# Performance work log

Measured on AMD Instinct MI355X. Metric: run time of the kernel, lower is better.

Reference implementation:

```python
import jax, jax.numpy as jnp
import numpy as np


def setup_inputs() -> dict:
    key = jax.random.key(0)
    x = jax.random.normal(key, (16, 2048, 64), dtype=jnp.float32)
    return {"x": x, "pred_len": 720, "k": 16, "low_freq": 1}


def reference(x, pred_len, k, low_freq):
    # x: (b, t, d); t assumed even (matches torch branch x_freq[:, low_freq:-1])
    b, t, d = x.shape
    x_freq = jnp.fft.rfft(x, axis=1)[:, low_freq:-1]          # (b, F, d) complex
    f = jnp.fft.rfftfreq(t).astype(jnp.float32)[low_freq:-1]  # (F,)

    # top-k frequencies per (batch, channel) by magnitude
    mag = jnp.transpose(jnp.abs(x_freq), (0, 2, 1))           # (b, d, F)
    _, idx = jax.lax.top_k(mag, k)                            # (b, d, k)
    xf_sel = jnp.take_along_axis(jnp.transpose(x_freq, (0, 2, 1)), idx, axis=2)
    xf_sel = jnp.transpose(xf_sel, (0, 2, 1))                 # (b, k, d)
    f_sel = jnp.transpose(f[idx], (0, 2, 1))                  # (b, k, d)

    # extrapolate: append conjugate / negated-frequency pairs
    xf = jnp.concatenate([xf_sel, jnp.conj(xf_sel)], axis=1)  # (b, 2k, d)
    ff = jnp.concatenate([f_sel, -f_sel], axis=1)[:, :, None, :]   # (b, 2k, 1, d)
    t_val = jnp.arange(t + pred_len, dtype=jnp.float32)[None, None, :, None]
    amp = (jnp.abs(xf) / t)[:, :, None, :]                    # (b, 2k, 1, d)
    phase = jnp.angle(xf)[:, :, None, :]                      # (b, 2k, 1, d)
    x_time = amp * jnp.cos(2.0 * jnp.pi * ff * t_val + phase) # (b, 2k, t+pred_len, d)
    return x_time.sum(axis=1)                                 # (b, t+pred_len, d)
```

## Files before the change

### kernel.cpp

```cpp
#include <hip/hip_runtime.h>
#include <hip/hip_bf16.h>

#define B_SZ 16
#define T_SZ 2048
#define D_SZ 64
#define M_SZ 1024
#define K_SEL 16
#define TOUT 2768
#define TPT 8
#define TAUS_PER_BLOCK (4 * TPT)
#define NCHUNK ((TOUT + TAUS_PER_BLOCK - 1) / TAUS_PER_BLOCK)

__global__ __launch_bounds__(256) void transpose_kernel(
    const float* __restrict__ x, float* __restrict__ xT)
{
    __shared__ float tile[64][65];
    const int b    = blockIdx.y;
    const int t0   = blockIdx.x * 64;
    const int lane = threadIdx.x & 63;
    const int row4 = threadIdx.x >> 6;

    #pragma unroll
    for (int rr = 0; rr < 16; ++rr) {
        int r = rr * 4 + row4;
        tile[r][lane] = x[((size_t)b * T_SZ + t0 + r) * D_SZ + lane];
    }
    __syncthreads();
    #pragma unroll
    for (int rr = 0; rr < 16; ++rr) {
        int d = rr * 4 + row4;
        xT[((size_t)b * D_SZ + d) * T_SZ + t0 + lane] = tile[lane][d];
    }
}

__global__ __launch_bounds__(256) void fft_topk_kernel(
    const float* __restrict__ xT,
    int* __restrict__ sel_j,
    float* __restrict__ sel_re,
    float* __restrict__ sel_im)
{
    __shared__ float a_re[M_SZ], a_im[M_SZ];
    __shared__ float tw_re[M_SZ / 2], tw_im[M_SZ / 2];
    __shared__ float X_re[M_SZ], X_im[M_SZ];
    __shared__ float mag2[M_SZ];
    __shared__ float cand_v[64];
    __shared__ int   cand_j[64];

    const int bd   = blockIdx.x;
    const int tid  = threadIdx.x;
    const int lane = tid & 63;
    const int w    = tid >> 6;

    for (int k = tid; k < M_SZ / 2; k += 256) {
        float a = (float)k * (1.0f / 512.0f);
        tw_re[k] =  cospif(a);
        tw_im[k] = -sinpif(a);
    }

    const float2* xb2 = (const float2*)(xT + (size_t)bd * T_SZ);
    #pragma unroll
    for (int r = 0; r < 4; ++r) {
        int m = tid + 256 * r;
        float2 v = xb2[m];
        int pos = __brev((unsigned)m) >> 22;
        a_re[pos] = v.x;
        a_im[pos] = v.y;
    }
    __syncthreads();

    for (int s = 0; s < 10; ++s) {
        #pragma unroll 2
        for (int q = tid; q < M_SZ / 2; q += 256) {
            int half = 1 << s;
            int pos  = q & (half - 1);
            int i0   = ((q >> s) << (s + 1)) + pos;
            int i1   = i0 + half;
            int twi  = pos << (9 - s);
            float wr = tw_re[twi], wi = tw_im[twi];
            float br = a_re[i1],  bi = a_im[i1];
            float tr = fmaf(wr, br, -wi * bi);
            float ti = fmaf(wr, bi,  wi * br);
            float ar = a_re[i0],  ai = a_im[i0];
            a_re[i0] = ar + tr;  a_im[i0] = ai + ti;
            a_re[i1] = ar - tr;  a_im[i1] = ai - ti;
        }
        __syncthreads();
    }

    for (int j = tid; j < M_SZ; j += 256) {
        if (j == 0) {
            X_re[0] = 0.0f; X_im[0] = 0.0f; mag2[0] = -2.0f;
            continue;
        }
        int jc = M_SZ - j;
        float zr = a_re[j],  zi = a_im[j];
        float cr = a_re[jc], ci = a_im[jc];
        float er = 0.5f * (zr + cr), ei = 0.5f * (zi - ci);
        float ur = zr - cr,  vv = zi + ci;
        float orr = 0.5f * vv, oii = -0.5f * ur;
        float a  = (float)j * (1.0f / 1024.0f);
        float twr =  cospif(a);
        float twq = -sinpif(a);
        float xr = er + twr * orr - twq * oii;
        float xi = ei + twr * oii + twq * orr;
        X_re[j] = xr; X_im[j] = xi;
        mag2[j] = xr * xr + xi * xi;
    }
    __syncthreads();

    float v[4]; int jj[4];
    #pragma unroll
    for (int r = 0; r < 4; ++r) {
        jj[r] = w * 256 + r * 64 + lane;
        v[r]  = mag2[jj[r]];
    }
    float my_v = -3.0f; int my_j = 0;
    for (int it = 0; it < K_SEL; ++it) {
        float bv = -2.5f; int bj = 1 << 20;
        #pragma unroll
        for (int r = 0; r < 4; ++r)
            if (v[r] > bv) { bv = v[r]; bj = jj[r]; }
        #pragma unroll
        for (int off = 32; off; off >>= 1) {
            float ov = __shfl_xor(bv, off);
            int   oj = __shfl_xor(bj, off);
            if (ov > bv || (ov == bv && oj < bj)) { bv = ov; bj = oj; }
        }
        if (lane == it) { my_v = bv; my_j = bj; }
        #pragma unroll
        for (int r = 0; r < 4; ++r)
            if (jj[r] == bj) v[r] = -2.0f;
    }
    if (lane < K_SEL) { cand_v[w * K_SEL + lane] = my_v; cand_j[w * K_SEL + lane] = my_j; }
    __syncthreads();

    if (w == 0) {
        float cv = cand_v[lane]; int cj = cand_j[lane];
        int out_j = 0;
        for (int it = 0; it < K_SEL; ++it) {
            float rv = cv; int rj = cj;
            #pragma unroll
            for (int off = 32; off; off >>= 1) {
                float ov = __shfl_xor(rv, off);
                int   oj = __shfl_xor(rj, off);
                if (ov > rv || (ov == rv && oj < rj)) { rv = ov; rj = oj; }
            }
            if (lane == it) out_j = rj;
            if (cj == rj) cv = -2.0f;
        }
        if (lane < K_SEL) {
            int j = out_j;
            sel_j [bd * K_SEL + lane] = j;
            sel_re[bd * K_SEL + lane] = X_re[j];
            sel_im[bd * K_SEL + lane] = X_im[j];
        }
    }
}

__global__ __launch_bounds__(256) void synth_kernel(
    const int*   __restrict__ sel_j,
    const float* __restrict__ sel_re,
    const float* __restrict__ sel_im,
    float* __restrict__ out)
{
    const int bid   = blockIdx.x;
    const int b     = bid / NCHUNK;
    const int chunk = bid - b * NCHUNK;
    const int tid   = threadIdx.x;
    const int d     = tid & 63;
    const int tg    = tid >> 6;

    const int g = (b * D_SZ + d) * K_SEL;
    int   j [K_SEL];
    float re[K_SEL];
    float im[K_SEL];
    const int4*   pj = (const int4*)  (sel_j  + g);
    const float4* pr = (const float4*)(sel_re + g);
    const float4* pi = (const float4*)(sel_im + g);
    #pragma unroll
    for (int r = 0; r < 4; ++r) {
        int4   a = pj[r];
        float4 c = pr[r];
        float4 s = pi[r];
        j [4*r+0] = a.x; j [4*r+1] = a.y; j [4*r+2] = a.z; j [4*r+3] = a.w;
        re[4*r+0] = c.x; re[4*r+1] = c.y; re[4*r+2] = c.z; re[4*r+3] = c.w;
        im[4*r+0] = s.x; im[4*r+1] = s.y; im[4*r+2] = s.z; im[4*r+3] = s.w;
    }

    const int tau0 = chunk * TAUS_PER_BLOCK + tg * TPT;
    #pragma unroll
    for (int u = 0; u < TPT; ++u) {
        int tau = tau0 + u;
        if (tau >= TOUT) break;
        float acc = 0.0f;
        #pragma unroll
        for (int q = 0; q < K_SEL; ++q) {
            int   ph = (j[q] * tau) & (T_SZ - 1);
            float r  = (float)ph * (1.0f / (float)T_SZ);
            float c  = __builtin_amdgcn_cosf(r);
            float s  = __builtin_amdgcn_sinf(r);
            acc = fmaf(re[q], c, acc);
            acc = fmaf(-im[q], s, acc);
        }
        out[((size_t)b * TOUT + tau) * D_SZ + d] = acc * (1.0f / 1024.0f);
    }
}

extern "C" void kernel_launch(void* const* d_in, const int* in_sizes, int n_in,
                              void* d_out, int out_size, void* d_ws, size_t ws_size,
                              hipStream_t stream) {
    const float* x = (const float*)d_in[0];

    float* xT     = (float*)d_ws;
    char*  base   = (char*)d_ws + (size_t)B_SZ * T_SZ * D_SZ * 4;
    int*   sel_j  = (int*)base;
    float* sel_re = (float*)(base + (size_t)B_SZ * D_SZ * K_SEL * 4);
    float* sel_im = (float*)(base + (size_t)2 * B_SZ * D_SZ * K_SEL * 4);

    transpose_kernel<<<dim3(T_SZ / 64, B_SZ), dim3(256), 0, stream>>>(x, xT);

    fft_topk_kernel<<<dim3(B_SZ * D_SZ), dim3(256), 0, stream>>>(
        xT, sel_j, sel_re, sel_im);

    synth_kernel<<<dim3(B_SZ * NCHUNK), dim3(256), 0, stream>>>(
        sel_j, sel_re, sel_im, (float*)d_out);
}
```

Before: 117.2 us.

## Drop transpose kernel and use angle-recurrence rotation in synthesis

The separate transpose kernel is removed, and the FFT kernel now reads x directly with a stride of D between time samples. The synthesis kernel computes cos/sin once per frequency at the start of each tau run and then advances them with a complex-rotation recurrence, in place of evaluating sin/cos for every (tau, q). TPT is doubled to 16 so each recurrence covers more steps. The goal is to cut one launch, the extra global round trip, and transcendental work, at the cost of uncoalesced strided loads in the FFT and some accumulated rounding error over 16 recurrence steps.

Measured after the change: 110.0 us. 1.06x faster.

```diff
diff --git a/kernel.cpp b/kernel.cpp
--- a/kernel.cpp
+++ b/kernel.cpp
@@ -7,34 +7,12 @@
 #define M_SZ 1024
 #define K_SEL 16
 #define TOUT 2768
-#define TPT 8
+#define TPT 16
 #define TAUS_PER_BLOCK (4 * TPT)
 #define NCHUNK ((TOUT + TAUS_PER_BLOCK - 1) / TAUS_PER_BLOCK)
 
-__global__ __launch_bounds__(256) void transpose_kernel(
-    const float* __restrict__ x, float* __restrict__ xT)
-{
-    __shared__ float tile[64][65];
-    const int b    = blockIdx.y;
-    const int t0   = blockIdx.x * 64;
-    const int lane = threadIdx.x & 63;
-    const int row4 = threadIdx.x >> 6;
-
-    #pragma unroll
-    for (int rr = 0; rr < 16; ++rr) {
-        int r = rr * 4 + row4;
-        tile[r][lane] = x[((size_t)b * T_SZ + t0 + r) * D_SZ + lane];
-    }
-    __syncthreads();
-    #pragma unroll
-    for (int rr = 0; rr < 16; ++rr) {
-        int d = rr * 4 + row4;
-        xT[((size_t)b * D_SZ + d) * T_SZ + t0 + lane] = tile[lane][d];
-    }
-}
-
 __global__ __launch_bounds__(256) void fft_topk_kernel(
-    const float* __restrict__ xT,
+    const float* __restrict__ x,
     int* __restrict__ sel_j,
     float* __restrict__ sel_re,
     float* __restrict__ sel_im)
@@ -47,6 +25,8 @@
     __shared__ int   cand_j[64];
 
     const int bd   = blockIdx.x;
+    const int b    = bd >> 6;
+    const int d    = bd & 63;
     const int tid  = threadIdx.x;
     const int lane = tid & 63;
     const int w    = tid >> 6;
@@ -57,14 +37,15 @@
         tw_im[k] = -sinpif(a);
     }
 
-    const float2* xb2 = (const float2*)(xT + (size_t)bd * T_SZ);
+    const float* xb = x + (size_t)b * T_SZ * D_SZ + d;
     #pragma unroll
     for (int r = 0; r < 4; ++r) {
         int m = tid + 256 * r;
-        float2 v = xb2[m];
+        float xe = xb[(2 * m) * D_SZ];
+        float xo = xb[(2 * m + 1) * D_SZ];
         int pos = __brev((unsigned)m) >> 22;
-        a_re[pos] = v.x;
-        a_im[pos] = v.y;
+        a_re[pos] = xe;
+        a_im[pos] = xo;
     }
     __syncthreads();
 
@@ -170,6 +151,10 @@
     const int d     = tid & 63;
     const int tg    = tid >> 6;
 
+    const int tau0 = chunk * TAUS_PER_BLOCK + tg * TPT;
+    if (tau0 >= TOUT) return;
+    const int nu = (TOUT - tau0 < TPT) ? (TOUT - tau0) : TPT;
+
     const int g = (b * D_SZ + d) * K_SEL;
     int   j [K_SEL];
     float re[K_SEL];
@@ -187,22 +172,33 @@
         im[4*r+0] = s.x; im[4*r+1] = s.y; im[4*r+2] = s.z; im[4*r+3] = s.w;
     }
 
-    const int tau0 = chunk * TAUS_PER_BLOCK + tg * TPT;
+    float acc[TPT];
+    #pragma unroll
+    for (int u = 0; u < TPT; ++u) acc[u] = 0.0f;
+
+    #pragma unroll
+    for (int q = 0; q < K_SEL; ++q) {
+        int   ph0 = (j[q] * tau0) & (T_SZ - 1);
+        float r0  = (float)ph0  * (1.0f / (float)T_SZ);
+        float rw  = (float)j[q] * (1.0f / (float)T_SZ);
+        float c   = __builtin_amdgcn_cosf(r0);
+        float s   = __builtin_amdgcn_sinf(r0);
+        float cw  = __builtin_amdgcn_cosf(rw);
+        float sw  = __builtin_amdgcn_sinf(rw);
+        #pragma unroll
+        for (int u = 0; u < TPT; ++u) {
+            acc[u] = fmaf(re[q], c, acc[u]);
+            acc[u] = fmaf(-im[q], s, acc[u]);
+            float cn = fmaf(c, cw, -s * sw);
+            float sn = fmaf(s, cw,  c * sw);
+            c = cn; s = sn;
+        }
+    }
+
+    float* ob = out + ((size_t)b * TOUT + tau0) * D_SZ + d;
     #pragma unroll
     for (int u = 0; u < TPT; ++u) {
-        int tau = tau0 + u;
-        if (tau >= TOUT) break;
-        float acc = 0.0f;
-        #pragma unroll
-        for (int q = 0; q < K_SEL; ++q) {
-            int   ph = (j[q] * tau) & (T_SZ - 1);
-            float r  = (float)ph * (1.0f / (float)T_SZ);
-            float c  = __builtin_amdgcn_cosf(r);
-            float s  = __builtin_amdgcn_sinf(r);
-            acc = fmaf(re[q], c, acc);
-            acc = fmaf(-im[q], s, acc);
-        }
-        out[((size_t)b * TOUT + tau) * D_SZ + d] = acc * (1.0f / 1024.0f);
+        if (u < nu) ob[(size_t)u * D_SZ] = acc[u] * (1.0f / 1024.0f);
     }
 }
 
@@ -211,16 +207,12 @@
                               hipStream_t stream) {
     const float* x = (const float*)d_in[0];
 
-    float* xT     = (float*)d_ws;
-    char*  base   = (char*)d_ws + (size_t)B_SZ * T_SZ * D_SZ * 4;
-    int*   sel_j  = (int*)base;
-    float* sel_re = (float*)(base + (size_t)B_SZ * D_SZ * K_SEL * 4);
-    float* sel_im = (float*)(base + (size_t)2 * B_SZ * D_SZ * K_SEL * 4);
-
-    transpose_kernel<<<dim3(T_SZ / 64, B_SZ), dim3(256), 0, stream>>>(x, xT);
+    int*   sel_j  = (int*)d_ws;
+    float* sel_re = (float*)((char*)d_ws + (size_t)B_SZ * D_SZ * K_SEL * 4);
+    float* sel_im = (float*)((char*)d_ws + (size_t)2 * B_SZ * D_SZ * K_SEL * 4);
 
     fft_topk_kernel<<<dim3(B_SZ * D_SZ), dim3(256), 0, stream>>>(
-        xT, sel_j, sel_re, sel_im);
+        x, sel_j, sel_re, sel_im);
 
     synth_kernel<<<dim3(B_SZ * NCHUNK), dim3(256), 0, stream>>>(
         sel_j, sel_re, sel_im, (float*)d_out);
```
